# Kernel optimization log

Hardware: AMD Instinct MI355X
Metric: run time of the kernel (lower is better)

## Reference

```python
import jax, jax.numpy as jnp
import numpy as np

RES_SCALE = 0.1
B, C, H, W = 16, 256, 96, 96


def conv3x3(x, w):
    # NCHW input, OIHW weight, SAME padding (padding=1 for k=3), no bias
    return jax.lax.conv_general_dilated(
        x, w, window_strides=(1, 1), padding="SAME",
        dimension_numbers=("NCHW", "OIHW", "NCHW"))


def setup_inputs() -> dict:
    key = jax.random.key(0)
    k1, k2, k3, k4 = jax.random.split(key, 4)
    fan = C * 9
    x = jax.random.normal(k1, (B, C, H, W), dtype=jnp.float32)
    conv2_w = jax.random.normal(k2, (C, C, 3, 3), dtype=jnp.float32) / np.sqrt(fan)
    conv3_w = jax.random.normal(k3, (C, C, 3, 3), dtype=jnp.float32) / np.sqrt(fan)
    prelu_w = jnp.full((1,), 0.25, dtype=jnp.float32)  # nn.PReLU default init
    # interleaved channel partition: P=0::3 (86), R=1::3 (85), T=2::3 (85)
    idx_p = jnp.arange(0, C, 3, dtype=jnp.int32)
    idx_r = jnp.arange(1, C, 3, dtype=jnp.int32)
    idx_t = jnp.arange(2, C, 3, dtype=jnp.int32)
    return {"x": x, "conv2_w": conv2_w, "conv3_w": conv3_w, "prelu_w": prelu_w,
            "idx_p": idx_p, "idx_r": idx_r, "idx_t": idx_t}


def reference(x, conv2_w, conv3_w, prelu_w, idx_p, idx_r, idx_t):
    # op2 = conv2(prune(x, skip_gate)) ; all-ones gate -> identity prune
    op2 = conv3x3(x, conv2_w)  # [B, C, H, W]
    # per-channel activation routing (gathers permute channel order to [P,R,T])
    gp = op2[:, idx_p]                                  # [B, 86, H, W]
    a = jnp.concatenate([
        jnp.where(gp >= 0, gp, prelu_w[0] * gp),        # PReLU (1 shared param)
        jax.nn.relu(op2[:, idx_r]),                     # [B, 85, H, W]
        jnp.tanh(op2[:, idx_t]),                        # [B, 85, H, W]
    ], axis=1)                                          # [B, C, H, W]
    # conv_tot branch: op3 = conv3(a)*res_scale + x * reshape(skip_conv_gate)
    # skip_conv_gate == ones here, so the skip scaling is identity
    op3 = conv3x3(a, conv3_w) * RES_SCALE + x
    return op3


if __name__ == "__main__":
    out = reference(**setup_inputs())
    print(out.shape, out.dtype)
```

## Files before the change

kernel.cpp:

```cpp
#include <hip/hip_runtime.h>
#include <math.h>


#define Bn 16
#define Cn 256
#define Hn 96
#define Wn 96
#define PH 98
#define PW 98
#define HW (Hn*Wn)

typedef __bf16 bf16x8 __attribute__((ext_vector_type(8)));
typedef float  f32x4  __attribute__((ext_vector_type(4)));

__device__ __forceinline__ unsigned short f2bf(float f) {
    unsigned int u = __float_as_uint(f);
    unsigned int r = (u + 0x7fffu + ((u >> 16) & 1u)) >> 16;
    return (unsigned short)r;
}

__device__ __forceinline__ void lds_load16(void* lds, const void* g) {
    auto gp = (const __attribute__((address_space(1))) char*)(unsigned long long)(uintptr_t)g;
    auto lp = (__attribute__((address_space(3))) char*)(unsigned int)(uintptr_t)lds;
    __builtin_amdgcn_global_load_lds(gp, lp, 16, 0, 0);
}

#define SB() __builtin_amdgcn_sched_barrier(0)
#define MEMFENCE() asm volatile("" ::: "memory")

__global__ __launch_bounds__(256)
void zero_border_k(unsigned short* __restrict__ t) {
    int idx = blockIdx.x * 256 + threadIdx.x;
    int oct = idx & 31;
    int rest = idx >> 5;
    int pidx = rest % 388;
    int b = rest / 388;
    int h, w;
    if (pidx < 98)       { h = 0;  w = pidx; }
    else if (pidx < 196) { h = 97; w = pidx - 98; }
    else if (pidx < 292) { h = pidx - 196 + 1; w = 0; }
    else                 { h = pidx - 292 + 1; w = 97; }
    size_t e = ((size_t)(b * PH + h) * PW + w) * 256 + oct * 8;
    *(uint4*)(t + e) = make_uint4(0u, 0u, 0u, 0u);
}

template<bool PERM>
__global__ __launch_bounds__(256)
void pack_w_k(const float* __restrict__ w, unsigned short* __restrict__ wp) {
    int idx = blockIdx.x * 256 + threadIdx.x;
    int ci_l = idx & 31;
    int c    = (idx >> 5) & 255;
    int v    = idx >> 13;
    int k9   = v % 9;
    int cc   = v / 9;
    int co;
    if (PERM) {
        co = (c < 86) ? c * 3 : (c < 171) ? (c - 86) * 3 + 1 : (c - 171) * 3 + 2;
    } else {
        co = c;
    }
    float val = w[((size_t)co * 256 + cc * 32 + ci_l) * 9 + k9];
    wp[idx] = f2bf(val);
}

__global__ __launch_bounds__(256)
void transform_x_k(const float* __restrict__ x, unsigned short* __restrict__ xp) {
    __shared__ float s[32 * 33];
    const int t = threadIdx.x;
    const int col0 = blockIdx.x * 32;
    const int row  = blockIdx.y;
    const int z = blockIdx.z;
    const int b = z >> 3;
    const int ci0 = (z & 7) * 32;

    #pragma unroll
    for (int i = 0; i < 4; ++i) {
        int ci = i * 8 + (t >> 5);
        int px = t & 31;
        s[ci * 33 + px] = x[((size_t)(b * Cn + ci0 + ci)) * HW + row * Wn + col0 + px];
    }
    __syncthreads();
    const int px = t >> 3;
    const int c4 = (t & 7) * 4;
    ushort4 o;
    o.x = f2bf(s[(c4 + 0) * 33 + px]);
    o.y = f2bf(s[(c4 + 1) * 33 + px]);
    o.z = f2bf(s[(c4 + 2) * 33 + px]);
    o.w = f2bf(s[(c4 + 3) * 33 + px]);
    size_t e = ((size_t)(b * PH + row + 1) * PW + (col0 + px + 1)) * 256 + ci0 + c4;
    *(ushort4*)(xp + e) = o;
}

template<int MODE>
__global__ __launch_bounds__(512, 2)
void conv_k(const unsigned short* __restrict__ in_cl,
            const unsigned short* __restrict__ wp,
            const float* __restrict__ prelu_w,
            const float* __restrict__ xres,
            void* __restrict__ outp)
{
    __shared__ unsigned short s_x[2][2048 * 8];
    __shared__ unsigned short s_w[9 * 128 * 32];

    const int tid = threadIdx.x;
    const int bid = blockIdx.x;
    const int wg = (bid & 7) * 96 + (bid >> 3);
    const int blk_co = (wg & 1) * 128;
    const int t2 = wg >> 1;
    const int tile = t2 % 24;
    const int b = t2 / 24;
    const int R0 = (tile / 3) * 12;
    const int C0 = (tile % 3) * 32;

    const int lane = tid & 63;
    const int wv = tid >> 6;
    const int l15 = lane & 15;
    const int qq = lane >> 4;
    const int cg = wv & 1;
    const int wrow = wv >> 1;
    const int qa = qq ^ ((l15 >> 1) & 3);

    const unsigned short* img = in_cl + (size_t)b * PH * PW * 256;

    int xg[4];
    #pragma unroll
    for (int i = 0; i < 4; ++i) {
        int slot = i * 512 + tid;
        int lsl = slot ^ ((slot >> 3) & 3);
        if (lsl > 1903) lsl = 1903;
        int p = lsl >> 2;
        int pr = p / 34, pc = p - pr * 34;
        xg[i] = ((R0 + pr) * PW + (C0 + pc)) * 256 + (lsl & 3) * 8;
    }
    int wgo[9];
    #pragma unroll
    for (int i = 0; i < 9; ++i) {
        int slot = i * 512 + tid;
        int lsl = slot ^ ((slot >> 3) & 3);
        int k9 = lsl >> 9;
        int co = (lsl >> 2) & 127;
        wgo[i] = (k9 * 256 + blk_co + co) * 32 + (lsl & 3) * 8;
    }

    f32x4 acc[4][6];
    #pragma unroll
    for (int m = 0; m < 4; ++m)
        #pragma unroll
        for (int n = 0; n < 6; ++n) acc[m][n] = 0.f;

    #pragma unroll
    for (int i = 0; i < 4; ++i) lds_load16(&s_x[0][(size_t)(i * 512 + tid) * 8], img + xg[i]);
    #pragma unroll
    for (int i = 0; i < 9; ++i) lds_load16(&s_w[(size_t)(i * 512 + tid) * 8], wp + wgo[i]);
    MEMFENCE(); SB();
    #pragma unroll
    for (int i = 0; i < 4; ++i) lds_load16(&s_x[1][(size_t)(i * 512 + tid) * 8], img + xg[i] + 32);
    MEMFENCE(); SB();
    asm volatile("s_waitcnt vmcnt(4)" ::: "memory");
    SB();
    __builtin_amdgcn_s_barrier();
    SB();

#define LOADF(AF, BF, K) {                                                        \
    const int kh_ = (K) / 3, kw_ = (K) - 3 * kh_;                                 \
    _Pragma("unroll")                                                             \
    for (int m = 0; m < 4; ++m) {                                                 \
        const int row_ = (K) * 128 + cg * 64 + m * 16 + l15;                      \
        AF[m] = *(const bf16x8*)&s_w[row_ * 32 + qa * 8];                         \
    }                                                                             \
    _Pragma("unroll")                                                             \
    for (int n = 0; n < 6; ++n) {                                                 \
        const int P_ = (wrow * 3 + (n >> 1) + kh_) * 34 + (n & 1) * 16 + l15 + kw_; \
        BF[n] = *(const bf16x8*)&sxc[P_ * 32 + ((qq ^ ((P_ >> 1) & 3)) << 3)];    \
    }                                                                             \
}
#define MFMA_ON(AF, BF) {                                                         \
    _Pragma("unroll")                                                             \
    for (int n = 0; n < 6; ++n)                                                   \
        _Pragma("unroll")                                                         \
        for (int m = 0; m < 4; ++m)                                               \
            acc[m][n] = __builtin_amdgcn_mfma_f32_16x16x32_bf16(AF[m], BF[n], acc[m][n], 0, 0, 0); \
}

    for (int c = 0; c < 8; ++c) {
        const unsigned short* sxc = s_x[c & 1];
        __builtin_amdgcn_s_setprio(1);
        #pragma unroll
        for (int k9 = 0; k9 < 9; ++k9) {
            bf16x8 af[4], bf[6];
            LOADF(af, bf, k9);
            MFMA_ON(af, bf);
        }
        __builtin_amdgcn_s_setprio(0);

        if (c < 7) {
            __builtin_amdgcn_s_barrier();
            SB();
            #pragma unroll
            for (int i = 0; i < 9; ++i)
                lds_load16(&s_w[(size_t)(i * 512 + tid) * 8],
                           wp + (size_t)(c + 1) * 73728 + wgo[i]);
            MEMFENCE(); SB();
            if (c < 6) {
                #pragma unroll
                for (int i = 0; i < 4; ++i)
                    lds_load16(&s_x[c & 1][(size_t)(i * 512 + tid) * 8],
                               img + xg[i] + (c + 2) * 32);
                MEMFENCE(); SB();
                asm volatile("s_waitcnt vmcnt(4)" ::: "memory");
            } else {
                asm volatile("s_waitcnt vmcnt(0)" ::: "memory");
            }
            SB();
            __builtin_amdgcn_s_barrier();
            SB();
        }
    }
#undef LOADF
#undef MFMA_ON

    if constexpr (MODE == 0) {
        const float pw = prelu_w[0];
        unsigned short* aout = (unsigned short*)outp;
        #pragma unroll
        for (int n = 0; n < 6; ++n) {
            const int row_p = wrow * 3 + (n >> 1);
            const int col_p = (n & 1) * 16 + l15;
            size_t pix = ((size_t)(b * PH + R0 + row_p + 1)) * PW + (C0 + col_p + 1);
            #pragma unroll
            for (int m = 0; m < 4; ++m) {
                const int cb = blk_co + cg * 64 + m * 16 + qq * 4;
                float r[4];
                #pragma unroll
                for (int j = 0; j < 4; ++j) {
                    const int ch = cb + j;
                    float s = acc[m][n][j];
                    if (ch < 86)        r[j] = s >= 0.f ? s : pw * s;
                    else if (ch < 171)  r[j] = fmaxf(s, 0.f);
                    else {
                        float e = __expf(2.f * s);
                        r[j] = 1.f - 2.f / (e + 1.f);
                    }
                }
                ushort4 o;
                o.x = f2bf(r[0]); o.y = f2bf(r[1]); o.z = f2bf(r[2]); o.w = f2bf(r[3]);
                *(ushort4*)(aout + pix * 256 + cb) = o;
            }
        }
    } else {
        float* fout = (float*)outp;
        #pragma unroll
        for (int n = 0; n < 6; ++n) {
            const int row_p = wrow * 3 + (n >> 1);
            const int col_p = (n & 1) * 16 + l15;
            #pragma unroll
            for (int m = 0; m < 4; ++m) {
                const int cb = blk_co + cg * 64 + m * 16 + qq * 4;
                size_t base = ((size_t)(b * Cn + cb)) * HW + (size_t)(R0 + row_p) * Wn + (C0 + col_p);
                #pragma unroll
                for (int j = 0; j < 4; ++j)
                    fout[base + (size_t)j * HW] = acc[m][n][j] * 0.1f + xres[base + (size_t)j * HW];
            }
        }
    }
}

extern "C" void kernel_launch(void* const* d_in, const int* in_sizes, int n_in,
                              void* d_out, int out_size, void* d_ws, size_t ws_size,
                              hipStream_t stream) {
    const float* x  = (const float*)d_in[0];
    const float* w2 = (const float*)d_in[1];
    const float* w3 = (const float*)d_in[2];
    const float* pw = (const float*)d_in[3];
    float* out = (float*)d_out;
    char* ws = (char*)d_ws;

    unsigned short* a_cl = (unsigned short*)ws;
    unsigned short* wp2  = (unsigned short*)(ws + 78675968);
    unsigned short* wp3  = (unsigned short*)(ws + 78675968 + 1179648);
    unsigned short* x_pad = (unsigned short*)d_out;

    zero_border_k<<<776, 256, 0, stream>>>(x_pad);
    zero_border_k<<<776, 256, 0, stream>>>(a_cl);
    pack_w_k<true ><<<2304, 256, 0, stream>>>(w2, wp2);
    pack_w_k<false><<<2304, 256, 0, stream>>>(w3, wp3);
    transform_x_k<<<dim3(3, 96, 128), 256, 0, stream>>>(x, x_pad);

    conv_k<0><<<768, 512, 0, stream>>>(x_pad, wp2, pw, nullptr, (void*)a_cl);
    conv_k<1><<<768, 512, 0, stream>>>(a_cl, wp3, nullptr, x, (void*)out);
}
```

Before: 406.4 us.

## Double-buffer weights per kernel row and software-pipeline LDS fragment loads

The weight staging is split from one 9-tap chunk per channel block into 3-tap (one kernel row) chunks, double-buffered in LDS so the next chunk's global-to-LDS copy overlaps the current MFMAs instead of waiting at a barrier. Input staging moves to the middle kernel-row step, and LDS fragment loads for the next tap are interleaved with the MFMAs of the previous one. The change also cuts LDS use for weights and swaps the launch bounds for an explicit waves-per-EU attribute. The cost is three times as many barriers per channel block and more registers from holding two fragment sets live.

```diff
diff --git a/kernel.cpp b/kernel.cpp
--- a/kernel.cpp
+++ b/kernel.cpp
@@ -92,7 +92,7 @@
 }
 
 template<int MODE>
-__global__ __launch_bounds__(512, 2)
+__global__ __launch_bounds__(512) __attribute__((amdgpu_waves_per_eu(2, 2)))
 void conv_k(const unsigned short* __restrict__ in_cl,
             const unsigned short* __restrict__ wp,
             const float* __restrict__ prelu_w,
@@ -100,7 +100,7 @@
             void* __restrict__ outp)
 {
     __shared__ unsigned short s_x[2][2048 * 8];
-    __shared__ unsigned short s_w[9 * 128 * 32];
+    __shared__ unsigned short s_w[2][1536 * 8];
 
     const int tid = threadIdx.x;
     const int bid = blockIdx.x;
@@ -132,14 +132,14 @@
         int pr = p / 34, pc = p - pr * 34;
         xg[i] = ((R0 + pr) * PW + (C0 + pc)) * 256 + (lsl & 3) * 8;
     }
-    int wgo[9];
-    #pragma unroll
-    for (int i = 0; i < 9; ++i) {
+    int wbase[3];
+    #pragma unroll
+    for (int i = 0; i < 3; ++i) {
         int slot = i * 512 + tid;
         int lsl = slot ^ ((slot >> 3) & 3);
-        int k9 = lsl >> 9;
+        int kw = lsl >> 9;
         int co = (lsl >> 2) & 127;
-        wgo[i] = (k9 * 256 + blk_co + co) * 32 + (lsl & 3) * 8;
+        wbase[i] = kw * 8192 + (blk_co + co) * 32 + (lsl & 3) * 8;
     }
 
     f32x4 acc[4][6];
@@ -149,74 +149,82 @@
         for (int n = 0; n < 6; ++n) acc[m][n] = 0.f;
 
     #pragma unroll
+    for (int i = 0; i < 3; ++i) lds_load16(&s_w[0][(size_t)(i * 512 + tid) * 8], wp + wbase[i]);
+    #pragma unroll
     for (int i = 0; i < 4; ++i) lds_load16(&s_x[0][(size_t)(i * 512 + tid) * 8], img + xg[i]);
-    #pragma unroll
-    for (int i = 0; i < 9; ++i) lds_load16(&s_w[(size_t)(i * 512 + tid) * 8], wp + wgo[i]);
     MEMFENCE(); SB();
-    #pragma unroll
-    for (int i = 0; i < 4; ++i) lds_load16(&s_x[1][(size_t)(i * 512 + tid) * 8], img + xg[i] + 32);
-    MEMFENCE(); SB();
-    asm volatile("s_waitcnt vmcnt(4)" ::: "memory");
+    asm volatile("s_waitcnt vmcnt(0)" ::: "memory");
     SB();
     __builtin_amdgcn_s_barrier();
     SB();
 
-#define LOADF(AF, BF, K) {                                                        \
-    const int kh_ = (K) / 3, kw_ = (K) - 3 * kh_;                                 \
+#define LOADW(AF, KW) {                                                           \
     _Pragma("unroll")                                                             \
     for (int m = 0; m < 4; ++m) {                                                 \
-        const int row_ = (K) * 128 + cg * 64 + m * 16 + l15;                      \
-        AF[m] = *(const bf16x8*)&s_w[row_ * 32 + qa * 8];                         \
+        const int row_ = (KW) * 128 + cg * 64 + m * 16 + l15;                     \
+        AF[m] = *(const bf16x8*)&swc[row_ * 32 + qa * 8];                         \
     }                                                                             \
+}
+#define LOADX(BF, KW) {                                                           \
     _Pragma("unroll")                                                             \
     for (int n = 0; n < 6; ++n) {                                                 \
-        const int P_ = (wrow * 3 + (n >> 1) + kh_) * 34 + (n & 1) * 16 + l15 + kw_; \
+        const int P_ = (wrow * 3 + (n >> 1) + kh) * 34 + (n & 1) * 16 + l15 + (KW); \
         BF[n] = *(const bf16x8*)&sxc[P_ * 32 + ((qq ^ ((P_ >> 1) & 3)) << 3)];    \
     }                                                                             \
 }
 #define MFMA_ON(AF, BF) {                                                         \
+    __builtin_amdgcn_s_setprio(1);                                                \
     _Pragma("unroll")                                                             \
     for (int n = 0; n < 6; ++n)                                                   \
         _Pragma("unroll")                                                         \
         for (int m = 0; m < 4; ++m)                                               \
             acc[m][n] = __builtin_amdgcn_mfma_f32_16x16x32_bf16(AF[m], BF[n], acc[m][n], 0, 0, 0); \
-}
-
-    for (int c = 0; c < 8; ++c) {
+    __builtin_amdgcn_s_setprio(0);                                                \
+}
+
+    for (int s = 0; s < 24; ++s) {
+        const int c  = s / 3;
+        const int kh = s - 3 * c;
+        const unsigned short* swc = s_w[s & 1];
         const unsigned short* sxc = s_x[c & 1];
-        __builtin_amdgcn_s_setprio(1);
-        #pragma unroll
-        for (int k9 = 0; k9 < 9; ++k9) {
-            bf16x8 af[4], bf[6];
-            LOADF(af, bf, k9);
-            MFMA_ON(af, bf);
-        }
-        __builtin_amdgcn_s_setprio(0);
-
-        if (c < 7) {
-            __builtin_amdgcn_s_barrier();
-            SB();
-            #pragma unroll
-            for (int i = 0; i < 9; ++i)
-                lds_load16(&s_w[(size_t)(i * 512 + tid) * 8],
-                           wp + (size_t)(c + 1) * 73728 + wgo[i]);
+        const bool stage_x = (kh == 1) && (c < 7);
+
+        if (s < 23) {
+            #pragma unroll
+            for (int i = 0; i < 3; ++i)
+                lds_load16(&s_w[(s + 1) & 1][(size_t)(i * 512 + tid) * 8],
+                           wp + (size_t)(s + 1) * 24576 + wbase[i]);
             MEMFENCE(); SB();
-            if (c < 6) {
-                #pragma unroll
-                for (int i = 0; i < 4; ++i)
-                    lds_load16(&s_x[c & 1][(size_t)(i * 512 + tid) * 8],
-                               img + xg[i] + (c + 2) * 32);
-                MEMFENCE(); SB();
-                asm volatile("s_waitcnt vmcnt(4)" ::: "memory");
-            } else {
-                asm volatile("s_waitcnt vmcnt(0)" ::: "memory");
-            }
-            SB();
-            __builtin_amdgcn_s_barrier();
-            SB();
-        }
-    }
-#undef LOADF
+        }
+        if (stage_x) {
+            #pragma unroll
+            for (int i = 0; i < 4; ++i)
+                lds_load16(&s_x[(c + 1) & 1][(size_t)(i * 512 + tid) * 8],
+                           img + xg[i] + (c + 1) * 32);
+            MEMFENCE(); SB();
+        }
+
+        {
+            bf16x8 afA[4], bfA[6], afB[4], bfB[6];
+            LOADW(afA, 0); LOADX(bfA, 0);
+            LOADW(afB, 1); LOADX(bfB, 1);
+            MFMA_ON(afA, bfA);
+            LOADW(afA, 2); LOADX(bfA, 2);
+            MFMA_ON(afB, bfB);
+            MFMA_ON(afA, bfA);
+        }
+
+        if (stage_x) {
+            asm volatile("s_waitcnt vmcnt(4)" ::: "memory");
+        } else {
+            asm volatile("s_waitcnt vmcnt(0)" ::: "memory");
+        }
+        SB();
+        __builtin_amdgcn_s_barrier();
+        SB();
+    }
+#undef LOADW
+#undef LOADX
 #undef MFMA_ON
 
     if constexpr (MODE == 0) {
```

Result: no change. 405.6 us (-0.2%).
